# Kernel optimization log

Measured on AMD Instinct MI355X. Metric: run time of the kernel, lower is better.

## Reference

```python
import jax, jax.numpy as jnp
import numpy as np

B, T, IMG, PS, D, DEPTH, NH = 1, 8, 224, 16, 768, 12, 12
HP = IMG // PS
NP = HP * HP          # 196 patches per frame
N = NP + 1            # +1 cls token per frame
DH = D // NH
MLP = 4 * D
SCALE = DH ** -0.5


def _ln(x, g, b):
    mu = x.mean(-1, keepdims=True)
    var = ((x - mu) ** 2).mean(-1, keepdims=True)
    return (x - mu) / jnp.sqrt(var + 1e-5) * g + b


def _forward(x, W_patch, b_patch, cls_token, pos_embed,
             ln1_g, ln1_b, qkv_w, qkv_b, proj_w, proj_b,
             ln2_g, ln2_b, fc1_w, fc1_b, fc2_w, fc2_b, lnf_g, lnf_b):
    Bc = x.shape[0]
    # --- patch embed (Conv3d k=(1,ps,ps), stride=(1,ps,ps) == per-frame patch matmul) ---
    p = x.reshape(Bc, T, 3, HP, PS, HP, PS).transpose(0, 1, 3, 5, 2, 4, 6)
    p = p.reshape(Bc, T, NP, 3 * PS * PS)
    emb = p @ W_patch.T + b_patch                     # [B,T,NP,D] (correct layout)
    # replicate torch flatten(3)/transpose(1,2)/reshape axis scramble:
    emb = jnp.swapaxes(emb, 2, 3).reshape(Bc, T, NP, D)
    cls = jnp.broadcast_to(cls_token.reshape(1, 1, 1, D), (Bc, T, 1, D))
    h = jnp.concatenate([cls, emb], axis=2) + pos_embed.reshape(1, 1, N, D)
    h = h.reshape(Bc, T * N, D)

    for i in range(DEPTH):
        # --- attention ---
        a = _ln(h, ln1_g[i], ln1_b[i])
        qkv = (a @ qkv_w[i] + qkv_b[i]).reshape(Bc, T * N, 3, NH, DH)
        q, k, v = (jnp.transpose(qkv[:, :, j], (0, 2, 1, 3)) for j in range(3))  # [B,H,S,dh]
        if i % 2 == 0:  # divided space-time
            qf = q.reshape(Bc, NH, T, N, DH)
            kf = k.reshape(Bc, NH, T, N, DH)
            vf = v.reshape(Bc, NH, T, N, DH)
            q_t = qf.mean(3, keepdims=True)           # [B,H,T,1,dh]
            k_t = kf.mean(3, keepdims=True)
            v_t = vf.mean(3, keepdims=True)
            attn_t = jax.nn.softmax(jnp.einsum('bhtqd,bhtkd->bhtqk', q_t, k_t) * SCALE, -1)
            x_t = jnp.einsum('bhtqk,bhtkd->bhtqd', attn_t, v_t)[:, :, :, 0]  # [B,H,T,dh]
            attn_s = jax.nn.softmax(jnp.einsum('bhtqd,bhtkd->bhtqk', qf, kf) * SCALE, -1)
            x_s = jnp.einsum('bhtqk,bhtkd->bhtqd', attn_s, vf)               # [B,H,T,N,dh]
            o = (x_s + x_t[:, :, :, None, :]).reshape(Bc, NH, T * N, DH)
        else:  # joint space-time
            attn = jax.nn.softmax(jnp.einsum('bhqd,bhkd->bhqk', q, k) * SCALE, -1)
            o = jnp.einsum('bhqk,bhkd->bhqd', attn, v)
        o = jnp.transpose(o, (0, 2, 1, 3)).reshape(Bc, T * N, D)
        h = h + (o @ proj_w[i] + proj_b[i])
        # --- mlp ---
        m = _ln(h, ln2_g[i], ln2_b[i])
        m = jax.nn.gelu(m @ fc1_w[i] + fc1_b[i], approximate=False)
        h = h + (m @ fc2_w[i] + fc2_b[i])

    return _ln(h, lnf_g, lnf_b).reshape(Bc, T, N, D)


def setup_inputs() -> dict:
    key = jax.random.key(0)
    ks = jax.random.split(key, 12)
    s = 0.02
    return {
        'x': jax.random.normal(ks[0], (B, T, 3, IMG, IMG), jnp.float32),
        'W_patch': jax.random.normal(ks[1], (D, 3 * PS * PS), jnp.float32) * s,
        'b_patch': jnp.zeros((D,), jnp.float32),
        'cls_token': jax.random.normal(ks[2], (1, 1, D), jnp.float32) * s,
        'pos_embed': jax.random.normal(ks[3], (1, N, D), jnp.float32) * s,
        'ln1_g': jnp.ones((DEPTH, D), jnp.float32),
        'ln1_b': jnp.zeros((DEPTH, D), jnp.float32),
        'qkv_w': jax.random.normal(ks[4], (DEPTH, D, 3 * D), jnp.float32) * s,
        'qkv_b': jnp.zeros((DEPTH, 3 * D), jnp.float32),
        'proj_w': jax.random.normal(ks[5], (DEPTH, D, D), jnp.float32) * s,
        'proj_b': jnp.zeros((DEPTH, D), jnp.float32),
        'ln2_g': jnp.ones((DEPTH, D), jnp.float32),
        'ln2_b': jnp.zeros((DEPTH, D), jnp.float32),
        'fc1_w': jax.random.normal(ks[6], (DEPTH, D, MLP), jnp.float32) * s,
        'fc1_b': jnp.zeros((DEPTH, MLP), jnp.float32),
        'fc2_w': jax.random.normal(ks[7], (DEPTH, MLP, D), jnp.float32) * s,
        'fc2_b': jnp.zeros((DEPTH, D), jnp.float32),
        'lnf_g': jnp.ones((D,), jnp.float32),
        'lnf_b': jnp.zeros((D,), jnp.float32),
    }


def reference(x, W_patch, b_patch, cls_token, pos_embed,
              ln1_g, ln1_b, qkv_w, qkv_b, proj_w, proj_b,
              ln2_g, ln2_b, fc1_w, fc1_b, fc2_w, fc2_b, lnf_g, lnf_b):
    return _forward(x, W_patch, b_patch, cls_token, pos_embed,
                    ln1_g, ln1_b, qkv_w, qkv_b, proj_w, proj_b,
                    ln2_g, ln2_b, fc1_w, fc1_b, fc2_w, fc2_b, lnf_g, lnf_b)
```

## Files before the change

kernel.cpp:

```cpp
#include <hip/hip_runtime.h>
#include <math.h>

#define Dm 768
#define Tn 8
#define Nn 197
#define Sn 1576
#define MLPn 3072
#define NPn 196
#define MPAD 1664

typedef unsigned short u16;
typedef __bf16 bf16x8 __attribute__((ext_vector_type(8)));
typedef float f32x4 __attribute__((ext_vector_type(4)));
typedef unsigned int u32x4 __attribute__((ext_vector_type(4)));
typedef u16 u16x8 __attribute__((ext_vector_type(8)));
typedef u16 u16x4 __attribute__((ext_vector_type(4)));

__device__ inline u16 f2bf(float f) {
    union { float f; unsigned u; } v; v.f = f;
    unsigned r = v.u + 0x7fffu + ((v.u >> 16) & 1u);
    return (u16)(r >> 16);
}
__device__ inline float bf2f(u16 v) {
    union { unsigned u; float f; } x; x.u = ((unsigned)v) << 16; return x.f;
}

__global__ __launch_bounds__(256) void im2col_k(const float* __restrict__ x, u16* __restrict__ P) {
    int idx = blockIdx.x * 256 + threadIdx.x;
    if (idx >= 1568 * 768) return;
    int c = idx % 768, r = idx / 768;
    int p = r % 196, t = r / 196;
    int hp = p / 14, wp = p % 14;
    int ch = c / 256, rem = c % 256, py = rem / 16, px = rem % 16;
    P[idx] = f2bf(x[((t * 3 + ch) * 224 + hp * 16 + py) * 224 + wp * 16 + px]);
}

__global__ __launch_bounds__(256) void cvt_k(const float* __restrict__ s, u16* __restrict__ d, int n) {
    int i = blockIdx.x * 256 + threadIdx.x;
    if (i < n) d[i] = f2bf(s[i]);
}

__global__ __launch_bounds__(256) void cvtT_layer_k(const float* __restrict__ qw, const float* __restrict__ pw,
                                                    const float* __restrict__ f1w, const float* __restrict__ f2w,
                                                    u16* __restrict__ Wq, u16* __restrict__ Wp,
                                                    u16* __restrict__ W1, u16* __restrict__ W2) {
    __shared__ float tile[32][33];
    int bid = blockIdx.x;
    const float* src; u16* dst; int K, N, k0, n0;
    if (bid < 1728)      { src = qw;  dst = Wq; K = 768;  N = 2304; int r = bid;        k0 = (r / 72) * 32; n0 = (r % 72) * 32; }
    else if (bid < 2304) { src = pw;  dst = Wp; K = 768;  N = 768;  int r = bid - 1728; k0 = (r / 24) * 32; n0 = (r % 24) * 32; }
    else if (bid < 4608) { src = f1w; dst = W1; K = 768;  N = 3072; int r = bid - 2304; k0 = (r / 96) * 32; n0 = (r % 96) * 32; }
    else                 { src = f2w; dst = W2; K = 3072; N = 768;  int r = bid - 4608; k0 = (r / 24) * 32; n0 = (r % 24) * 32; }
    int tx = threadIdx.x & 31, ty = threadIdx.x >> 5;
#pragma unroll
    for (int i = 0; i < 4; ++i) tile[ty + 8 * i][tx] = src[(size_t)(k0 + ty + 8 * i) * N + n0 + tx];
    __syncthreads();
#pragma unroll
    for (int i = 0; i < 4; ++i) dst[(size_t)(n0 + ty + 8 * i) * K + k0 + tx] = f2bf(tile[tx][ty + 8 * i]);
}

__global__ __launch_bounds__(256) void build_h_k(const float* __restrict__ emb, const float* __restrict__ cls,
                                                 const float* __restrict__ pos, float* __restrict__ h) {
    int idx = blockIdx.x * 256 + threadIdx.x;
    if (idx >= Sn * Dm) return;
    int d = idx % Dm, s = idx / Dm;
    int t = s / Nn, r = s % Nn;
    float v;
    if (r == 0) v = cls[d];
    else {
        int f = (r - 1) * Dm + d;
        int p = f % NPn, dd = f / NPn;
        v = emb[(size_t)(t * NPn + p) * Dm + dd];
    }
    h[idx] = v + pos[r * Dm + d];
}

template <typename OutT>
__global__ __launch_bounds__(256) void ln_k(const float* __restrict__ X, const float* __restrict__ g,
                                            const float* __restrict__ bta, OutT* __restrict__ Y) {
    int row = blockIdx.x;
    const float* x = X + (size_t)row * Dm;
    float s = 0.f, s2 = 0.f;
#pragma unroll
    for (int q = 0; q < 3; ++q) {
        float v = x[threadIdx.x + q * 256];
        s += v; s2 += v * v;
    }
#pragma unroll
    for (int off = 1; off < 64; off <<= 1) {
        s  += __shfl_xor(s,  off);
        s2 += __shfl_xor(s2, off);
    }
    __shared__ float red[8];
    int wv = threadIdx.x >> 6;
    if ((threadIdx.x & 63) == 0) { red[wv * 2] = s; red[wv * 2 + 1] = s2; }
    __syncthreads();
    s  = red[0] + red[2] + red[4] + red[6];
    s2 = red[1] + red[3] + red[5] + red[7];
    float mu  = s * (1.f / 768.f);
    float var = s2 * (1.f / 768.f) - mu * mu;
    float rstd = rsqrtf(var + 1e-5f);
#pragma unroll
    for (int q = 0; q < 3; ++q) {
        int i = threadIdx.x + q * 256;
        float v = (x[i] - mu) * rstd * g[i] + bta[i];
        if constexpr (sizeof(OutT) == 2) Y[(size_t)row * Dm + i] = f2bf(v);
        else                             Y[(size_t)row * Dm + i] = v;
    }
}

__global__ __launch_bounds__(256) void mgemm_k(const u16* __restrict__ A, const u16* __restrict__ Bt,
                                               float* __restrict__ Cp, int N, int Kfull, int Kc) {
    __shared__ u16 As[4096];
    __shared__ u16 Bs[4096];
    int split = blockIdx.z;
    A  += split * Kc;
    Bt += split * Kc;
    Cp += (size_t)split * MPAD * N;
    int tid = threadIdx.x;
    int lane = tid & 63, w = tid >> 6;
    int wm = w & 1, wn = w >> 1;
    int m0 = blockIdx.y * 128, n0 = blockIdx.x * 128;
    f32x4 acc[4][4] = {};
    int c0 = tid, c1 = tid + 256;
    int ar0 = ((c0 >> 6) << 4) + (c0 & 15), ac0 = ((c0 >> 4) & 3) << 3;
    int ar1 = ((c1 >> 6) << 4) + (c1 & 15), ac1 = ((c1 >> 4) & 3) << 3;
    const u16* Arow0 = A  + (size_t)(m0 + ar0) * Kfull + ac0;
    const u16* Arow1 = A  + (size_t)(m0 + ar1) * Kfull + ac1;
    const u16* Brow0 = Bt + (size_t)(n0 + ar0) * Kfull + ac0;
    const u16* Brow1 = Bt + (size_t)(n0 + ar1) * Kfull + ac1;
    for (int k0 = 0; k0 < Kc; k0 += 32) {
        u32x4 a0 = *(const u32x4*)(Arow0 + k0);
        u32x4 a1 = *(const u32x4*)(Arow1 + k0);
        u32x4 b0 = *(const u32x4*)(Brow0 + k0);
        u32x4 b1 = *(const u32x4*)(Brow1 + k0);
        *(u32x4*)(As + c0 * 8) = a0;
        *(u32x4*)(As + c1 * 8) = a1;
        *(u32x4*)(Bs + c0 * 8) = b0;
        *(u32x4*)(Bs + c1 * 8) = b1;
        __syncthreads();
        bf16x8 af[4], bfr[4];
#pragma unroll
        for (int i = 0; i < 4; ++i) {
            af[i]  = *(const bf16x8*)(As + (((wm * 4 + i) * 64 + lane) << 3));
            bfr[i] = *(const bf16x8*)(Bs + (((wn * 4 + i) * 64 + lane) << 3));
        }
#pragma unroll
        for (int mi = 0; mi < 4; ++mi)
#pragma unroll
            for (int ni = 0; ni < 4; ++ni)
                acc[mi][ni] = __builtin_amdgcn_mfma_f32_16x16x32_bf16(af[mi], bfr[ni], acc[mi][ni], 0, 0, 0);
        __syncthreads();
    }
    int rbase = (lane >> 4) << 2, cl = lane & 15;
#pragma unroll
    for (int mi = 0; mi < 4; ++mi)
#pragma unroll
        for (int r = 0; r < 4; ++r) {
            int gm = m0 + wm * 64 + mi * 16 + rbase + r;
#pragma unroll
            for (int ni = 0; ni < 4; ++ni) {
                int gn = n0 + wn * 64 + ni * 16 + cl;
                Cp[(size_t)gm * N + gn] = acc[mi][ni][r];
            }
        }
}

template <bool GELU_ACT, bool RESID, typename OutT>
__global__ __launch_bounds__(256) void ep_k(const float* __restrict__ Cp, const float* __restrict__ bias,
                                            const float* __restrict__ resid, OutT* __restrict__ out,
                                            int N, int S) {
    int row = blockIdx.y;
    int n = blockIdx.x * 1024 + threadIdx.x * 4;
    if (n >= N) return;
    size_t off = (size_t)row * N + n;
    f32x4 acc = *(const f32x4*)(Cp + off);
    for (int s = 1; s < S; ++s)
        acc += *(const f32x4*)(Cp + (size_t)s * MPAD * N + off);
    acc += *(const f32x4*)(bias + n);
    if (GELU_ACT) {
#pragma unroll
        for (int j = 0; j < 4; ++j) acc[j] = 0.5f * acc[j] * (1.f + erff(acc[j] * 0.7071067811865476f));
    }
    if (RESID) acc += *(const f32x4*)(resid + off);
    if constexpr (sizeof(OutT) == 2) {
        u16x4 o;
#pragma unroll
        for (int j = 0; j < 4; ++j) o[j] = f2bf(acc[j]);
        *(u16x4*)((u16*)out + off) = o;
    } else {
        *(f32x4*)((float*)out + off) = acc;
    }
}

__global__ __launch_bounds__(64) void vmean_k(const u16* __restrict__ qkv, float* __restrict__ vm) {
    int g = blockIdx.x;
    int h = g >> 3, t = g & 7;
    int d = threadIdx.x;
    float s = 0.f;
    for (int n = 0; n < Nn; ++n)
        s += bf2f(qkv[(size_t)(t * Nn + n) * 2304 + 1536 + h * 64 + d]);
    vm[g * 64 + d] = s * (1.f / 197.f);
}

__global__ __launch_bounds__(256) void attn_mfma_k(const u16* __restrict__ qkv, float* __restrict__ Ou,
                                                   float* __restrict__ ml, int even, int nsplit,
                                                   int NG, int Sq) {
    __shared__ __align__(16) u16 Ks[64 * 64];
    __shared__ __align__(16) u16 Vt[64 * 64];
    __shared__ __align__(16) u16 Ps[4 * 32 * 64];
    int g = blockIdx.y;
    int h, sbase;
    if (even) { h = g >> 3; sbase = (g & 7) * Nn; } else { h = g; sbase = 0; }
    int split = blockIdx.z;
    int chunk = (Sq + nsplit - 1) / nsplit;
    int kbeg = split * chunk, kend = min(Sq, kbeg + chunk);
    int tid = threadIdx.x, lane = tid & 63, w = tid >> 6;
    int quad = lane >> 4, l15 = lane & 15;
    int q0w = blockIdx.x * 128 + w * 32;
    u16* Pw = Ps + w * 2048;

    bf16x8 aq[2][2];
#pragma unroll
    for (int mb = 0; mb < 2; ++mb) {
        int qidx = q0w + mb * 16 + l15; if (qidx >= Sq) qidx = Sq - 1;
        const u16* qp = qkv + (size_t)(sbase + qidx) * 2304 + h * 64;
#pragma unroll
        for (int ks = 0; ks < 2; ++ks)
            aq[mb][ks] = *(const bf16x8*)(qp + ks * 32 + quad * 8);
    }
    f32x4 acc_o[2][4] = {};
    float m_run[2][4], l_run[2][4];
#pragma unroll
    for (int mb = 0; mb < 2; ++mb)
#pragma unroll
        for (int r = 0; r < 4; ++r) { m_run[mb][r] = -INFINITY; l_run[mb][r] = 0.f; }

    for (int kt = kbeg; kt < kend; kt += 64) {
        int cnt = kend - kt; if (cnt > 64) cnt = 64;
        {
            int dc = tid & 7;
#pragma unroll
            for (int p = 0; p < 2; ++p) {
                int row = (tid >> 3) + 32 * p;
                u32x4 kd = {};
                if (row < cnt) kd = *(const u32x4*)(qkv + (size_t)(sbase + kt + row) * 2304 + 768 + h * 64 + dc * 8);
                *(u32x4*)(Ks + row * 64 + ((dc ^ (row & 7)) << 3)) = kd;
            }
        }
        {
            int d = (tid & 31) * 2, kc = tid >> 5;
            u16x8 lo, hi;
#pragma unroll
            for (int i = 0; i < 8; ++i) {
                int key = kc * 8 + i;
                unsigned t = 0;
                if (key < cnt) t = *(const unsigned*)(qkv + (size_t)(sbase + kt + key) * 2304 + 1536 + h * 64 + d);
                lo[i] = (u16)(t & 0xffffu); hi[i] = (u16)(t >> 16);
            }
            *(u16x8*)(Vt + d * 64 + ((kc ^ (d & 7)) << 3)) = lo;
            *(u16x8*)(Vt + (d + 1) * 64 + ((kc ^ ((d + 1) & 7)) << 3)) = hi;
        }
        __syncthreads();
        f32x4 acc_s[2][4] = {};
#pragma unroll
        for (int ni = 0; ni < 4; ++ni) {
            int key = l15 + ni * 16;
#pragma unroll
            for (int ks = 0; ks < 2; ++ks) {
                bf16x8 bk = *(const bf16x8*)(Ks + key * 64 + ((((ks << 2) + quad) ^ (key & 7)) << 3));
                acc_s[0][ni] = __builtin_amdgcn_mfma_f32_16x16x32_bf16(aq[0][ks], bk, acc_s[0][ni], 0, 0, 0);
                acc_s[1][ni] = __builtin_amdgcn_mfma_f32_16x16x32_bf16(aq[1][ks], bk, acc_s[1][ni], 0, 0, 0);
            }
        }
#pragma unroll
        for (int mb = 0; mb < 2; ++mb) {
#pragma unroll
            for (int ni = 0; ni < 4; ++ni) {
                int keyabs = kt + l15 + ni * 16;
#pragma unroll
                for (int r = 0; r < 4; ++r) {
                    float sv = acc_s[mb][ni][r] * 0.125f;
                    if (keyabs >= kend) sv = -1e30f;
                    acc_s[mb][ni][r] = sv;
                }
            }
#pragma unroll
            for (int r = 0; r < 4; ++r) {
                float mx = fmaxf(fmaxf(acc_s[mb][0][r], acc_s[mb][1][r]), fmaxf(acc_s[mb][2][r], acc_s[mb][3][r]));
                mx = fmaxf(mx, __shfl_xor(mx, 1));
                mx = fmaxf(mx, __shfl_xor(mx, 2));
                mx = fmaxf(mx, __shfl_xor(mx, 4));
                mx = fmaxf(mx, __shfl_xor(mx, 8));
                float mnew = fmaxf(m_run[mb][r], mx);
                float pv[4], ps = 0.f;
#pragma unroll
                for (int ni = 0; ni < 4; ++ni) { pv[ni] = __expf(acc_s[mb][ni][r] - mnew); ps += pv[ni]; }
                ps += __shfl_xor(ps, 1);
                ps += __shfl_xor(ps, 2);
                ps += __shfl_xor(ps, 4);
                ps += __shfl_xor(ps, 8);
                float alpha = __expf(m_run[mb][r] - mnew);
                l_run[mb][r] = l_run[mb][r] * alpha + ps;
                m_run[mb][r] = mnew;
#pragma unroll
                for (int ni = 0; ni < 4; ++ni) acc_o[mb][ni][r] *= alpha;
                int prow = mb * 16 + quad * 4 + r;
#pragma unroll
                for (int ni = 0; ni < 4; ++ni) {
                    int key = l15 + ni * 16;
                    Pw[prow * 64 + (((key >> 3) ^ (prow & 7)) << 3) + (key & 7)] = f2bf(pv[ni]);
                }
            }
        }
        bf16x8 ap[2][2];
#pragma unroll
        for (int mb = 0; mb < 2; ++mb)
#pragma unroll
            for (int ks = 0; ks < 2; ++ks)
                ap[mb][ks] = *(const bf16x8*)(Pw + (mb * 16 + l15) * 64 + ((((ks << 2) + quad) ^ (l15 & 7)) << 3));
#pragma unroll
        for (int ni = 0; ni < 4; ++ni) {
            int d = l15 + ni * 16;
#pragma unroll
            for (int ks = 0; ks < 2; ++ks) {
                bf16x8 bv = *(const bf16x8*)(Vt + d * 64 + ((((ks << 2) + quad) ^ (d & 7)) << 3));
                acc_o[0][ni] = __builtin_amdgcn_mfma_f32_16x16x32_bf16(ap[0][ks], bv, acc_o[0][ni], 0, 0, 0);
                acc_o[1][ni] = __builtin_amdgcn_mfma_f32_16x16x32_bf16(ap[1][ks], bv, acc_o[1][ni], 0, 0, 0);
            }
        }
        __syncthreads();
    }
    size_t gb = ((size_t)split * NG + g) * Sq;
#pragma unroll
    for (int mb = 0; mb < 2; ++mb)
#pragma unroll
        for (int r = 0; r < 4; ++r) {
            int q = q0w + mb * 16 + quad * 4 + r;
            if (q < Sq) {
                float* op = Ou + (gb + q) * 64;
#pragma unroll
                for (int ni = 0; ni < 4; ++ni) op[l15 + ni * 16] = acc_o[mb][ni][r];
                if (l15 == 0) {
                    ml[(gb + q) * 2]     = m_run[mb][r];
                    ml[(gb + q) * 2 + 1] = l_run[mb][r];
                }
            }
        }
}

__global__ __launch_bounds__(256) void comb_k(const float* __restrict__ Ou, const float* __restrict__ ml,
                                              const float* __restrict__ vm, u16* __restrict__ ob,
                                              int even, int nsplit, int NG, int Sq) {
    int g = blockIdx.y;
    int q = blockIdx.x * 4 + (threadIdx.x >> 6);
    int d = threadIdx.x & 63;
    if (q >= Sq) return;
    int h, sbase;
    if (even) { h = g >> 3; sbase = (g & 7) * Nn; } else { h = g; sbase = 0; }
    float M = -INFINITY;
    for (int s = 0; s < nsplit; ++s) M = fmaxf(M, ml[(((size_t)s * NG + g) * Sq + q) * 2]);
    float num = 0.f, den = 0.f;
    for (int s = 0; s < nsplit; ++s) {
        size_t base = ((size_t)s * NG + g) * Sq + q;
        float wgt = __expf(ml[base * 2] - M);
        den += wgt * ml[base * 2 + 1];
        num += wgt * Ou[base * 64 + d];
    }
    float o = num / den;
    if (even) o += vm[g * 64 + d];
    ob[(size_t)(sbase + q) * Dm + h * 64 + d] = f2bf(o);
}

extern "C" void kernel_launch(void* const* d_in, const int* in_sizes, int n_in,
                              void* d_out, int out_size, void* d_ws, size_t ws_size,
                              hipStream_t stream) {
    (void)in_sizes; (void)n_in; (void)out_size; (void)ws_size;
    const float* x       = (const float*)d_in[0];
    const float* W_patch = (const float*)d_in[1];
    const float* b_patch = (const float*)d_in[2];
    const float* cls     = (const float*)d_in[3];
    const float* pos     = (const float*)d_in[4];
    const float* ln1_g   = (const float*)d_in[5];
    const float* ln1_b   = (const float*)d_in[6];
    const float* qkv_w   = (const float*)d_in[7];
    const float* qkv_b   = (const float*)d_in[8];
    const float* proj_w  = (const float*)d_in[9];
    const float* proj_b  = (const float*)d_in[10];
    const float* ln2_g   = (const float*)d_in[11];
    const float* ln2_b   = (const float*)d_in[12];
    const float* fc1_w   = (const float*)d_in[13];
    const float* fc1_b   = (const float*)d_in[14];
    const float* fc2_w   = (const float*)d_in[15];
    const float* fc2_b   = (const float*)d_in[16];
    const float* lnf_g   = (const float*)d_in[17];
    const float* lnf_b   = (const float*)d_in[18];

    char* base = (char*)d_ws;
    auto alloc = [&](size_t bytes) { void* p = base; base += (bytes + 255) & ~(size_t)255; return p; };
    u16*   P    = (u16*)  alloc((size_t)MPAD * 768 * 2);
    u16*   Wq   = (u16*)  alloc((size_t)2304 * 768 * 2);
    u16*   Wp   = (u16*)  alloc((size_t)768 * 768 * 2);
    u16*   W1   = (u16*)  alloc((size_t)3072 * 768 * 2);
    u16*   W2   = (u16*)  alloc((size_t)768 * 3072 * 2);
    float* emb  = (float*)alloc((size_t)1568 * 768 * 4);
    float* h    = (float*)alloc((size_t)Sn * Dm * 4);
    u16*   a    = (u16*)  alloc((size_t)MPAD * 768 * 2);
    u16*   qkvb = (u16*)  alloc((size_t)Sn * 2304 * 2);
    u16*   ob   = (u16*)  alloc((size_t)MPAD * 768 * 2);
    u16*   mb   = (u16*)  alloc((size_t)MPAD * 3072 * 2);
    float* vm   = (float*)alloc((size_t)96 * 64 * 4);
    float* Ou   = (float*)alloc((size_t)3 * 12 * Sn * 64 * 4);
    float* ml   = (float*)alloc((size_t)3 * 12 * Sn * 2 * 4);
    float* Cp   = (float*)alloc((size_t)3 * MPAD * 2304 * 4);

    im2col_k<<<(1568 * 768 + 255) / 256, 256, 0, stream>>>(x, P);
    cvt_k<<<(768 * 768 + 255) / 256, 256, 0, stream>>>(W_patch, Wp, 768 * 768);
    mgemm_k<<<dim3(6, 13, 3), 256, 0, stream>>>(P, Wp, Cp, 768, 768, 256);
    ep_k<false, false, float><<<dim3(1, 1568), 256, 0, stream>>>(Cp, b_patch, nullptr, emb, 768, 3);
    build_h_k<<<(Sn * Dm + 255) / 256, 256, 0, stream>>>(emb, cls, pos, h);

    for (int i = 0; i < 12; ++i) {
        cvtT_layer_k<<<6912, 256, 0, stream>>>(
            qkv_w + (size_t)i * 768 * 2304, proj_w + (size_t)i * 768 * 768,
            fc1_w + (size_t)i * 768 * 3072, fc2_w + (size_t)i * 3072 * 768,
            Wq, Wp, W1, W2);
        ln_k<u16><<<Sn, 256, 0, stream>>>(h, ln1_g + i * Dm, ln1_b + i * Dm, a);
        mgemm_k<<<dim3(18, 13, 3), 256, 0, stream>>>(a, Wq, Cp, 2304, 768, 256);
        ep_k<false, false, u16><<<dim3(3, Sn), 256, 0, stream>>>(Cp, qkv_b + i * 2304, nullptr, qkvb, 2304, 3);
        if ((i & 1) == 0) {
            vmean_k<<<96, 64, 0, stream>>>(qkvb, vm);
            attn_mfma_k<<<dim3(2, 96, 1), 256, 0, stream>>>(qkvb, Ou, ml, 1, 1, 96, Nn);
            comb_k<<<dim3(50, 96), 256, 0, stream>>>(Ou, ml, vm, ob, 1, 1, 96, Nn);
        } else {
            attn_mfma_k<<<dim3(13, 12, 3), 256, 0, stream>>>(qkvb, Ou, ml, 0, 3, 12, Sn);
            comb_k<<<dim3(394, 12), 256, 0, stream>>>(Ou, ml, vm, ob, 0, 3, 12, Sn);
        }
        mgemm_k<<<dim3(6, 13, 4), 256, 0, stream>>>(ob, Wp, Cp, 768, 768, 192);
        ep_k<false, true, float><<<dim3(1, Sn), 256, 0, stream>>>(Cp, proj_b + i * Dm, h, h, 768, 4);
        ln_k<u16><<<Sn, 256, 0, stream>>>(h, ln2_g + i * Dm, ln2_b + i * Dm, a);
        mgemm_k<<<dim3(24, 13, 2), 256, 0, stream>>>(a, W1, Cp, 3072, 768, 384);
        ep_k<true, false, u16><<<dim3(3, Sn), 256, 0, stream>>>(Cp, fc1_b + i * MLPn, nullptr, mb, 3072, 2);
        mgemm_k<<<dim3(6, 13, 4), 256, 0, stream>>>(mb, W2, Cp, 768, 3072, 768);
        ep_k<false, true, float><<<dim3(1, Sn), 256, 0, stream>>>(Cp, fc2_b + i * Dm, h, h, 768, 4);
    }
    ln_k<float><<<Sn, 256, 0, stream>>>(h, lnf_g, lnf_b, (float*)d_out);
}
```

Before: 2.439 ms.

## Fuse GEMM epilogues, drop split-K, and convert all layer weights in one launch

Folds bias, GELU and residual add into the GEMM epilogue, which removes the separate epilogue kernels and the fp32 split-K partial buffers they read. The GEMM is templated on tile size: 128x128 tiles for the wide QKV and FC1 GEMMs, 64x64 tiles for the N=768 GEMMs so there are enough blocks without split-K. All twelve layers' weight transposes and bf16 conversions now run in one launch up front instead of one launch per layer. This costs more workspace memory, and FC2 loses its K parallelism since it now runs the full K=3072 loop in each block.

```diff
diff --git a/kernel.cpp b/kernel.cpp
--- a/kernel.cpp
+++ b/kernel.cpp
@@ -40,17 +40,19 @@
     if (i < n) d[i] = f2bf(s[i]);
 }
 
-__global__ __launch_bounds__(256) void cvtT_layer_k(const float* __restrict__ qw, const float* __restrict__ pw,
-                                                    const float* __restrict__ f1w, const float* __restrict__ f2w,
-                                                    u16* __restrict__ Wq, u16* __restrict__ Wp,
-                                                    u16* __restrict__ W1, u16* __restrict__ W2) {
+__global__ __launch_bounds__(256) void cvtT_all_k(const float* __restrict__ qw, const float* __restrict__ pw,
+                                                  const float* __restrict__ f1w, const float* __restrict__ f2w,
+                                                  u16* __restrict__ Wq, u16* __restrict__ Wp,
+                                                  u16* __restrict__ W1, u16* __restrict__ W2) {
     __shared__ float tile[32][33];
-    int bid = blockIdx.x;
+    int layer = blockIdx.x / 6912;
+    int bid = blockIdx.x % 6912;
+    size_t lw = (size_t)layer * 768;
     const float* src; u16* dst; int K, N, k0, n0;
-    if (bid < 1728)      { src = qw;  dst = Wq; K = 768;  N = 2304; int r = bid;        k0 = (r / 72) * 32; n0 = (r % 72) * 32; }
-    else if (bid < 2304) { src = pw;  dst = Wp; K = 768;  N = 768;  int r = bid - 1728; k0 = (r / 24) * 32; n0 = (r % 24) * 32; }
-    else if (bid < 4608) { src = f1w; dst = W1; K = 768;  N = 3072; int r = bid - 2304; k0 = (r / 96) * 32; n0 = (r % 96) * 32; }
-    else                 { src = f2w; dst = W2; K = 3072; N = 768;  int r = bid - 4608; k0 = (r / 24) * 32; n0 = (r % 24) * 32; }
+    if (bid < 1728)      { src = qw  + lw * 2304; dst = Wq + lw * 2304; K = 768;  N = 2304; int r = bid;        k0 = (r / 72) * 32; n0 = (r % 72) * 32; }
+    else if (bid < 2304) { src = pw  + lw * 768;  dst = Wp + lw * 768;  K = 768;  N = 768;  int r = bid - 1728; k0 = (r / 24) * 32; n0 = (r % 24) * 32; }
+    else if (bid < 4608) { src = f1w + lw * 3072; dst = W1 + lw * 3072; K = 768;  N = 3072; int r = bid - 2304; k0 = (r / 96) * 32; n0 = (r % 96) * 32; }
+    else                 { src = f2w + lw * 3072; dst = W2 + lw * 3072; K = 3072; N = 768;  int r = bid - 4608; k0 = (r / 24) * 32; n0 = (r % 24) * 32; }
     int tx = threadIdx.x & 31, ty = threadIdx.x >> 5;
 #pragma unroll
     for (int i = 0; i < 4; ++i) tile[ty + 8 * i][tx] = src[(size_t)(k0 + ty + 8 * i) * N + n0 + tx];
@@ -109,87 +111,73 @@
     }
 }
 
+template <int BM, int BN, bool BIAS, bool GELU_ACT, bool RESID, typename OutT>
 __global__ __launch_bounds__(256) void mgemm_k(const u16* __restrict__ A, const u16* __restrict__ Bt,
-                                               float* __restrict__ Cp, int N, int Kfull, int Kc) {
-    __shared__ u16 As[4096];
-    __shared__ u16 Bs[4096];
-    int split = blockIdx.z;
-    A  += split * Kc;
-    Bt += split * Kc;
-    Cp += (size_t)split * MPAD * N;
-    int tid = threadIdx.x;
-    int lane = tid & 63, w = tid >> 6;
+                                               const float* __restrict__ bias, const float* __restrict__ resid,
+                                               OutT* __restrict__ out, int M, int N, int K) {
+    constexpr int FM = BM / 32, FN = BN / 32;
+    constexpr int CA = BM / 64, CB = BN / 64;
+    __shared__ u16 As[BM * 32];
+    __shared__ u16 Bs[BN * 32];
+    int tid = threadIdx.x, lane = tid & 63, w = tid >> 6;
     int wm = w & 1, wn = w >> 1;
-    int m0 = blockIdx.y * 128, n0 = blockIdx.x * 128;
-    f32x4 acc[4][4] = {};
-    int c0 = tid, c1 = tid + 256;
-    int ar0 = ((c0 >> 6) << 4) + (c0 & 15), ac0 = ((c0 >> 4) & 3) << 3;
-    int ar1 = ((c1 >> 6) << 4) + (c1 & 15), ac1 = ((c1 >> 4) & 3) << 3;
-    const u16* Arow0 = A  + (size_t)(m0 + ar0) * Kfull + ac0;
-    const u16* Arow1 = A  + (size_t)(m0 + ar1) * Kfull + ac1;
-    const u16* Brow0 = Bt + (size_t)(n0 + ar0) * Kfull + ac0;
-    const u16* Brow1 = Bt + (size_t)(n0 + ar1) * Kfull + ac1;
-    for (int k0 = 0; k0 < Kc; k0 += 32) {
-        u32x4 a0 = *(const u32x4*)(Arow0 + k0);
-        u32x4 a1 = *(const u32x4*)(Arow1 + k0);
-        u32x4 b0 = *(const u32x4*)(Brow0 + k0);
-        u32x4 b1 = *(const u32x4*)(Brow1 + k0);
-        *(u32x4*)(As + c0 * 8) = a0;
-        *(u32x4*)(As + c1 * 8) = a1;
-        *(u32x4*)(Bs + c0 * 8) = b0;
-        *(u32x4*)(Bs + c1 * 8) = b1;
+    int quad = lane >> 4, l15 = lane & 15;
+    int m0 = blockIdx.y * BM, n0 = blockIdx.x * BN;
+    f32x4 acc[FM][FN] = {};
+    const u16* Ap[CA];
+    const u16* Bp[CB];
+#pragma unroll
+    for (int i = 0; i < CA; ++i) {
+        int c = tid + 256 * i, row = ((c >> 6) << 4) + (c & 15), kc = (c >> 4) & 3;
+        Ap[i] = A + (size_t)(m0 + row) * K + kc * 8;
+    }
+#pragma unroll
+    for (int i = 0; i < CB; ++i) {
+        int c = tid + 256 * i, row = ((c >> 6) << 4) + (c & 15), kc = (c >> 4) & 3;
+        Bp[i] = Bt + (size_t)(n0 + row) * K + kc * 8;
+    }
+    for (int k0 = 0; k0 < K; k0 += 32) {
+        u32x4 av[CA], bv[CB];
+#pragma unroll
+        for (int i = 0; i < CA; ++i) av[i] = *(const u32x4*)(Ap[i] + k0);
+#pragma unroll
+        for (int i = 0; i < CB; ++i) bv[i] = *(const u32x4*)(Bp[i] + k0);
+#pragma unroll
+        for (int i = 0; i < CA; ++i) *(u32x4*)(As + (size_t)(tid + 256 * i) * 8) = av[i];
+#pragma unroll
+        for (int i = 0; i < CB; ++i) *(u32x4*)(Bs + (size_t)(tid + 256 * i) * 8) = bv[i];
         __syncthreads();
-        bf16x8 af[4], bfr[4];
-#pragma unroll
-        for (int i = 0; i < 4; ++i) {
-            af[i]  = *(const bf16x8*)(As + (((wm * 4 + i) * 64 + lane) << 3));
-            bfr[i] = *(const bf16x8*)(Bs + (((wn * 4 + i) * 64 + lane) << 3));
-        }
-#pragma unroll
-        for (int mi = 0; mi < 4; ++mi)
-#pragma unroll
-            for (int ni = 0; ni < 4; ++ni)
+        bf16x8 af[FM], bfr[FN];
+#pragma unroll
+        for (int i = 0; i < FM; ++i) af[i]  = *(const bf16x8*)(As + (((wm * FM + i) * 64 + lane) << 3));
+#pragma unroll
+        for (int i = 0; i < FN; ++i) bfr[i] = *(const bf16x8*)(Bs + (((wn * FN + i) * 64 + lane) << 3));
+#pragma unroll
+        for (int mi = 0; mi < FM; ++mi)
+#pragma unroll
+            for (int ni = 0; ni < FN; ++ni)
                 acc[mi][ni] = __builtin_amdgcn_mfma_f32_16x16x32_bf16(af[mi], bfr[ni], acc[mi][ni], 0, 0, 0);
         __syncthreads();
     }
-    int rbase = (lane >> 4) << 2, cl = lane & 15;
-#pragma unroll
-    for (int mi = 0; mi < 4; ++mi)
+#pragma unroll
+    for (int mi = 0; mi < FM; ++mi) {
 #pragma unroll
         for (int r = 0; r < 4; ++r) {
-            int gm = m0 + wm * 64 + mi * 16 + rbase + r;
-#pragma unroll
-            for (int ni = 0; ni < 4; ++ni) {
-                int gn = n0 + wn * 64 + ni * 16 + cl;
-                Cp[(size_t)gm * N + gn] = acc[mi][ni][r];
-            }
-        }
-}
-
-template <bool GELU_ACT, bool RESID, typename OutT>
-__global__ __launch_bounds__(256) void ep_k(const float* __restrict__ Cp, const float* __restrict__ bias,
-                                            const float* __restrict__ resid, OutT* __restrict__ out,
-                                            int N, int S) {
-    int row = blockIdx.y;
-    int n = blockIdx.x * 1024 + threadIdx.x * 4;
-    if (n >= N) return;
-    size_t off = (size_t)row * N + n;
-    f32x4 acc = *(const f32x4*)(Cp + off);
-    for (int s = 1; s < S; ++s)
-        acc += *(const f32x4*)(Cp + (size_t)s * MPAD * N + off);
-    acc += *(const f32x4*)(bias + n);
-    if (GELU_ACT) {
-#pragma unroll
-        for (int j = 0; j < 4; ++j) acc[j] = 0.5f * acc[j] * (1.f + erff(acc[j] * 0.7071067811865476f));
-    }
-    if (RESID) acc += *(const f32x4*)(resid + off);
-    if constexpr (sizeof(OutT) == 2) {
-        u16x4 o;
-#pragma unroll
-        for (int j = 0; j < 4; ++j) o[j] = f2bf(acc[j]);
-        *(u16x4*)((u16*)out + off) = o;
-    } else {
-        *(f32x4*)((float*)out + off) = acc;
+            int gm = m0 + wm * (FM * 16) + mi * 16 + (quad << 2) + r;
+            if (gm < M) {
+#pragma unroll
+                for (int ni = 0; ni < FN; ++ni) {
+                    int gn = n0 + wn * (FN * 16) + ni * 16 + l15;
+                    float v = acc[mi][ni][r];
+                    if (BIAS) v += bias[gn];
+                    if (GELU_ACT) v = 0.5f * v * (1.f + erff(v * 0.7071067811865476f));
+                    size_t off = (size_t)gm * N + gn;
+                    if (RESID) v += resid[off];
+                    if constexpr (sizeof(OutT) == 2) ((u16*)out)[off] = f2bf(v);
+                    else                             ((float*)out)[off] = v;
+                }
+            }
+        }
     }
 }
 
@@ -399,10 +387,11 @@
     char* base = (char*)d_ws;
     auto alloc = [&](size_t bytes) { void* p = base; base += (bytes + 255) & ~(size_t)255; return p; };
     u16*   P    = (u16*)  alloc((size_t)MPAD * 768 * 2);
-    u16*   Wq   = (u16*)  alloc((size_t)2304 * 768 * 2);
-    u16*   Wp   = (u16*)  alloc((size_t)768 * 768 * 2);
-    u16*   W1   = (u16*)  alloc((size_t)3072 * 768 * 2);
-    u16*   W2   = (u16*)  alloc((size_t)768 * 3072 * 2);
+    u16*   Wpa  = (u16*)  alloc((size_t)768 * 768 * 2);
+    u16*   Wq   = (u16*)  alloc((size_t)12 * 2304 * 768 * 2);
+    u16*   Wp   = (u16*)  alloc((size_t)12 * 768 * 768 * 2);
+    u16*   W1   = (u16*)  alloc((size_t)12 * 3072 * 768 * 2);
+    u16*   W2   = (u16*)  alloc((size_t)12 * 768 * 3072 * 2);
     float* emb  = (float*)alloc((size_t)1568 * 768 * 4);
     float* h    = (float*)alloc((size_t)Sn * Dm * 4);
     u16*   a    = (u16*)  alloc((size_t)MPAD * 768 * 2);
@@ -412,22 +401,19 @@
     float* vm   = (float*)alloc((size_t)96 * 64 * 4);
     float* Ou   = (float*)alloc((size_t)3 * 12 * Sn * 64 * 4);
     float* ml   = (float*)alloc((size_t)3 * 12 * Sn * 2 * 4);
-    float* Cp   = (float*)alloc((size_t)3 * MPAD * 2304 * 4);
 
     im2col_k<<<(1568 * 768 + 255) / 256, 256, 0, stream>>>(x, P);
-    cvt_k<<<(768 * 768 + 255) / 256, 256, 0, stream>>>(W_patch, Wp, 768 * 768);
-    mgemm_k<<<dim3(6, 13, 3), 256, 0, stream>>>(P, Wp, Cp, 768, 768, 256);
-    ep_k<false, false, float><<<dim3(1, 1568), 256, 0, stream>>>(Cp, b_patch, nullptr, emb, 768, 3);
+    cvt_k<<<(768 * 768 + 255) / 256, 256, 0, stream>>>(W_patch, Wpa, 768 * 768);
+    cvtT_all_k<<<12 * 6912, 256, 0, stream>>>(qkv_w, proj_w, fc1_w, fc2_w, Wq, Wp, W1, W2);
+
+    mgemm_k<64, 64, true, false, false, float><<<dim3(12, 25), 256, 0, stream>>>(
+        P, Wpa, b_patch, nullptr, emb, 1568, 768, 768);
     build_h_k<<<(Sn * Dm + 255) / 256, 256, 0, stream>>>(emb, cls, pos, h);
 
     for (int i = 0; i < 12; ++i) {
-        cvtT_layer_k<<<6912, 256, 0, stream>>>(
-            qkv_w + (size_t)i * 768 * 2304, proj_w + (size_t)i * 768 * 768,
-            fc1_w + (size_t)i * 768 * 3072, fc2_w + (size_t)i * 3072 * 768,
-            Wq, Wp, W1, W2);
         ln_k<u16><<<Sn, 256, 0, stream>>>(h, ln1_g + i * Dm, ln1_b + i * Dm, a);
-        mgemm_k<<<dim3(18, 13, 3), 256, 0, stream>>>(a, Wq, Cp, 2304, 768, 256);
-        ep_k<false, false, u16><<<dim3(3, Sn), 256, 0, stream>>>(Cp, qkv_b + i * 2304, nullptr, qkvb, 2304, 3);
+        mgemm_k<128, 128, true, false, false, u16><<<dim3(18, 13), 256, 0, stream>>>(
+            a, Wq + (size_t)i * 2304 * 768, qkv_b + i * 2304, nullptr, qkvb, Sn, 2304, 768);
         if ((i & 1) == 0) {
             vmean_k<<<96, 64, 0, stream>>>(qkvb, vm);
             attn_mfma_k<<<dim3(2, 96, 1), 256, 0, stream>>>(qkvb, Ou, ml, 1, 1, 96, Nn);
@@ -436,13 +422,13 @@
             attn_mfma_k<<<dim3(13, 12, 3), 256, 0, stream>>>(qkvb, Ou, ml, 0, 3, 12, Sn);
             comb_k<<<dim3(394, 12), 256, 0, stream>>>(Ou, ml, vm, ob, 0, 3, 12, Sn);
         }
-        mgemm_k<<<dim3(6, 13, 4), 256, 0, stream>>>(ob, Wp, Cp, 768, 768, 192);
-        ep_k<false, true, float><<<dim3(1, Sn), 256, 0, stream>>>(Cp, proj_b + i * Dm, h, h, 768, 4);
+        mgemm_k<64, 64, true, false, true, float><<<dim3(12, 25), 256, 0, stream>>>(
+            ob, Wp + (size_t)i * 768 * 768, proj_b + i * Dm, h, h, Sn, 768, 768);
         ln_k<u16><<<Sn, 256, 0, stream>>>(h, ln2_g + i * Dm, ln2_b + i * Dm, a);
-        mgemm_k<<<dim3(24, 13, 2), 256, 0, stream>>>(a, W1, Cp, 3072, 768, 384);
-        ep_k<true, false, u16><<<dim3(3, Sn), 256, 0, stream>>>(Cp, fc1_b + i * MLPn, nullptr, mb, 3072, 2);
-        mgemm_k<<<dim3(6, 13, 4), 256, 0, stream>>>(mb, W2, Cp, 768, 3072, 768);
-        ep_k<false, true, float><<<dim3(1, Sn), 256, 0, stream>>>(Cp, fc2_b + i * Dm, h, h, 768, 4);
+        mgemm_k<128, 128, true, true, false, u16><<<dim3(24, 13), 256, 0, stream>>>(
+            a, W1 + (size_t)i * 3072 * 768, fc1_b + i * MLPn, nullptr, mb, Sn, 3072, 768);
+        mgemm_k<64, 64, true, false, true, float><<<dim3(12, 25), 256, 0, stream>>>(
+            mb, W2 + (size_t)i * 768 * 3072, fc2_b + i * Dm, h, h, Sn, 768, 3072);
     }
     ln_k<float><<<Sn, 256, 0, stream>>>(h, lnf_g, lnf_b, (float*)d_out);
 }
```

Result: slower. 2.898 ms (+18.8%).
